# Performance work log

Hardware: AMD Instinct MI355X
Metric: run time of the kernel (lower is better)

## Reference

```python
import math
import jax, jax.numpy as jnp
import numpy as np

B, T, D_MODEL, N_HEADS = 2, 2048, 1024, 16
HEAD_DIM = D_MODEL // N_HEADS  # 64


def setup_inputs() -> dict:
    key = jax.random.key(0)
    k1, k2, k3, k4, k5 = jax.random.split(key, 5)
    x = jax.random.normal(k1, (B, T, D_MODEL), dtype=jnp.float32)
    init = 0.02
    Wq = jax.random.normal(k2, (D_MODEL, D_MODEL), dtype=jnp.float32) * init
    Wk = jax.random.normal(k3, (D_MODEL, D_MODEL), dtype=jnp.float32) * init
    Wv = jax.random.normal(k4, (D_MODEL, D_MODEL), dtype=jnp.float32) * init
    Wo = jax.random.normal(k5, (D_MODEL, D_MODEL), dtype=jnp.float32) * init
    # causal mask, broadcastable over (B, H): 1 = keep, 0 = masked
    mask = jnp.tril(jnp.ones((T, T), dtype=jnp.int32))[None, None, :, :]
    return {"x": x, "Wq": Wq, "Wk": Wk, "Wv": Wv, "Wo": Wo, "mask": mask}


def ternary_weight(W):
    # BitNet-b1.58 style ternary quantization with straight-through estimator
    scale = jnp.mean(jnp.abs(W))
    Wt = jnp.round(jnp.clip(W / (scale + 1e-8), -1.0, 1.0)) * scale
    return W + jax.lax.stop_gradient(Wt - W)


def rope_cos_sin(seq_len, dim):
    inv_freq = 1.0 / (10000.0 ** (jnp.arange(0, dim, 2, dtype=jnp.float32) / dim))
    freqs = jnp.outer(jnp.arange(seq_len, dtype=jnp.float32), inv_freq)  # [T, dim/2]
    emb = jnp.concatenate([freqs, freqs], axis=-1)  # [T, dim]
    return jnp.cos(emb)[None, None, :, :], jnp.sin(emb)[None, None, :, :]


def rotate_half(x):
    h = x.shape[-1] // 2
    return jnp.concatenate([-x[..., h:], x[..., :h]], axis=-1)


def reference(x, Wq, Wk, Wv, Wo, mask):
    Bb, Tt, C = x.shape
    H, D = N_HEADS, HEAD_DIM
    # ternary-quantized projections (bias-free)
    q = (x @ ternary_weight(Wq).T).reshape(Bb, Tt, H, D).transpose(0, 2, 1, 3)
    k = (x @ ternary_weight(Wk).T).reshape(Bb, Tt, H, D).transpose(0, 2, 1, 3)
    v = (x @ ternary_weight(Wv).T).reshape(Bb, Tt, H, D).transpose(0, 2, 1, 3)
    cos, sin = rope_cos_sin(Tt, D)  # [1,1,T,D]
    q = q * cos + rotate_half(q) * sin
    k = k * cos + rotate_half(k) * sin
    att = jnp.einsum("bhqd,bhkd->bhqk", q, k) / math.sqrt(D)
    att = jnp.where(mask == 0, -jnp.inf, att)
    att = jax.nn.softmax(att, axis=-1)  # dropout omitted (eval mode, p effectively 0)
    y = jnp.einsum("bhqk,bhkd->bhqd", att, v)
    y = y.transpose(0, 2, 1, 3).reshape(Bb, Tt, C)
    return y @ ternary_weight(Wo).T
```

## Files before the change

kernel.cpp:

```cpp
#include <hip/hip_runtime.h>
#include <math.h>

using bf16x8  = __attribute__((ext_vector_type(8))) __bf16;
using floatx4 = __attribute__((ext_vector_type(4))) float;
using ushortx8 = __attribute__((ext_vector_type(8))) unsigned short;
using ushortx4 = __attribute__((ext_vector_type(4))) unsigned short;
typedef unsigned short u16;

__device__ __forceinline__ float bf2f(u16 u) {
  unsigned int x = ((unsigned int)u) << 16;
  return __builtin_bit_cast(float, x);
}
__device__ __forceinline__ u16 f2bf(float f) {
  unsigned int x = __builtin_bit_cast(unsigned int, f);
  x += 0x7FFFu + ((x >> 16) & 1u);
  return (u16)(x >> 16);
}
__device__ __forceinline__ float fexp2(float x) { return __builtin_amdgcn_exp2f(x); }
__device__ __forceinline__ unsigned cvtpk(float lo, float hi) {
  unsigned r;
  asm("v_cvt_pk_bf16_f32 %0, %1, %2" : "=v"(r) : "v"(lo), "v"(hi));
  return r;
}

#define GLDS16(SRC, DST)                                                        \
  __builtin_amdgcn_global_load_lds((const __attribute__((address_space(1))) void*)(SRC), \
                                   (__attribute__((address_space(3))) void*)(DST), 16, 0, 0)

__global__ __launch_bounds__(256) void cvt_kernel(const float* __restrict__ x, u16* __restrict__ xb) {
  int g = (blockIdx.x * 256 + threadIdx.x) * 8;
  float4 a = *(const float4*)(x + g);
  float4 b = *(const float4*)(x + g + 4);
  ushortx8 o;
  o[0] = f2bf(a.x); o[1] = f2bf(a.y); o[2] = f2bf(a.z); o[3] = f2bf(a.w);
  o[4] = f2bf(b.x); o[5] = f2bf(b.y); o[6] = f2bf(b.z); o[7] = f2bf(b.w);
  *(ushortx8*)(xb + g) = o;
}

__global__ __launch_bounds__(256) void absum_kernel(const float* W0, const float* W1,
                                                    const float* W2, const float* W3,
                                                    float* partials) {
  const float* W = (blockIdx.y == 0) ? W0 : (blockIdx.y == 1) ? W1 : (blockIdx.y == 2) ? W2 : W3;
  int tid = threadIdx.x;
  int base = blockIdx.x * 16384 + tid;
  float s = 0.f;
#pragma unroll
  for (int i = 0; i < 64; ++i) s += fabsf(W[base + i * 256]);
  __shared__ float red[256];
  red[tid] = s;
  __syncthreads();
  for (int off = 128; off > 0; off >>= 1) {
    if (tid < off) red[tid] += red[tid + off];
    __syncthreads();
  }
  if (tid == 0) partials[blockIdx.y * 64 + blockIdx.x] = red[0];
}

__global__ void scales_kernel(const float* partials, float* scales) {
  int w = threadIdx.x;
  if (w < 4) {
    float s = 0.f;
    for (int i = 0; i < 64; ++i) s += partials[w * 64 + i];
    scales[w] = s * (1.f / 1048576.f);
  }
}

__global__ __launch_bounds__(256) void quant_kernel(const float* W0, const float* W1,
                                                    const float* W2, const float* W3,
                                                    const float* scales, u16* Wt) {
  int w = blockIdx.y;
  const float* W = (w == 0) ? W0 : (w == 1) ? W1 : (w == 2) ? W2 : W3;
  u16* O = Wt + (size_t)w * (1u << 20);
  float s = scales[w] + 1e-8f;
  int e = (blockIdx.x * 256 + threadIdx.x) * 4;
  float4 v = *(const float4*)(W + e);
  ushortx4 o;
  o[0] = f2bf(rintf(fminf(fmaxf(v.x / s, -1.f), 1.f)));
  o[1] = f2bf(rintf(fminf(fmaxf(v.y / s, -1.f), 1.f)));
  o[2] = f2bf(rintf(fminf(fmaxf(v.z / s, -1.f), 1.f)));
  o[3] = f2bf(rintf(fminf(fmaxf(v.w / s, -1.f), 1.f)));
  *(ushortx4*)(O + e) = o;
}

__global__ __launch_bounds__(256) void gemm_qkv(const u16* __restrict__ A, const u16* __restrict__ Wt,
                                                u16* __restrict__ QKV, u16* __restrict__ vt,
                                                const float* __restrict__ scales) {
  const int K = 1024;
  __shared__ __align__(16) u16 As[128][64];
  __shared__ __align__(16) u16 Bs[64][64];
  int tid = threadIdx.x;
  int wave = tid >> 6, lane = tid & 63;
  int quad = lane >> 4, l16 = lane & 15;
  int flat = blockIdx.y * 32 + blockIdx.x;
  int swz = (flat & 7) * 192 + (flat >> 3);
  int bx = swz & 31, by = swz >> 5;
  int bm = bx * 128;
  int bnc = by * 64;
  int mat = bnc >> 10, bn = bnc & 1023;
  int wm = wave * 32;
  floatx4 acc[2][4] = {};
  const u16* ga = A  + (size_t)(bm + wave * 32 + (lane >> 3)) * K + (lane & 7) * 8;
  const u16* gb = Wt + (size_t)(bnc + wave * 16 + (lane >> 3)) * K + (lane & 7) * 8;
  for (int k0 = 0; k0 < K; k0 += 64) {
    __syncthreads();
#pragma unroll
    for (int i = 0; i < 4; ++i)
      GLDS16(ga + (size_t)i * 8 * K + k0, &As[wave * 32 + i * 8][0]);
#pragma unroll
    for (int i = 0; i < 2; ++i)
      GLDS16(gb + (size_t)i * 8 * K + k0, &Bs[wave * 16 + i * 8][0]);
    __syncthreads();
#pragma unroll
    for (int kk = 0; kk < 64; kk += 32) {
      bf16x8 a[2], b[4];
#pragma unroll
      for (int i = 0; i < 2; ++i)
        a[i] = __builtin_bit_cast(bf16x8, *(const ushortx8*)&As[wm + i * 16 + l16][kk + quad * 8]);
#pragma unroll
      for (int j = 0; j < 4; ++j)
        b[j] = __builtin_bit_cast(bf16x8, *(const ushortx8*)&Bs[j * 16 + l16][kk + quad * 8]);
#pragma unroll
      for (int i = 0; i < 2; ++i)
#pragma unroll
        for (int j = 0; j < 4; ++j)
          acc[i][j] = __builtin_amdgcn_mfma_f32_16x16x32_bf16(a[i], b[j], acc[i][j], 0, 0, 0);
    }
  }
  float sc = scales[mat];
  if (mat < 2) {
    u16* outp = QKV + (size_t)mat * (4u << 20);
    float qs = (mat == 0) ? 0.125f * 1.4426950408889634f : 1.0f;
    float inv0 = exp2f(-(float)l16 * (13.287712379549449f / 32.f));
    float inv1 = exp2f(-(float)(16 + l16) * (13.287712379549449f / 32.f));
#pragma unroll
    for (int i = 0; i < 2; ++i)
#pragma unroll
      for (int rg = 0; rg < 4; ++rg) {
        int row = bm + wm + i * 16 + quad * 4 + rg;
        float tf = (float)(row & 2047);
#pragma unroll
        for (int j = 0; j < 2; ++j) {
          float ang = tf * (j ? inv1 : inv0);
          float s = __sinf(ang), c = __cosf(ang);
          float v1 = acc[i][j][rg] * sc, v2 = acc[i][j + 2][rg] * sc;
          int col = bn + j * 16 + l16;
          outp[(size_t)row * 1024 + col]      = f2bf((v1 * c - v2 * s) * qs);
          outp[(size_t)row * 1024 + col + 32] = f2bf((v2 * c + v1 * s) * qs);
        }
      }
  } else {
    int h = bn >> 6;
#pragma unroll
    for (int i = 0; i < 2; ++i) {
      int row0 = bm + wm + i * 16 + quad * 4;
      int b = row0 >> 11, t0 = row0 & 2047;
#pragma unroll
      for (int j = 0; j < 4; ++j) {
        int d = j * 16 + l16;
        ushortx4 o;
#pragma unroll
        for (int rg = 0; rg < 4; ++rg) o[rg] = f2bf(acc[i][j][rg] * sc);
        *(ushortx4*)(vt + (size_t)((b * 16 + h) * 64 + d) * 2048 + t0) = o;
      }
    }
  }
}

__global__ __launch_bounds__(256) void gemm_out(const u16* __restrict__ A, const u16* __restrict__ B,
                                                float* __restrict__ C, const float* __restrict__ scale_ptr) {
  const int K = 1024, N = 1024;
  __shared__ __align__(16) u16 As[128][64];
  __shared__ __align__(16) u16 Bs[128][64];
  int tid = threadIdx.x;
  int wave = tid >> 6, lane = tid & 63;
  int quad = lane >> 4, l16 = lane & 15;
  int bm = blockIdx.x * 128, bn = blockIdx.y * 128;
  int wm = (wave >> 1) * 64, wn = (wave & 1) * 64;
  floatx4 acc[4][4] = {};
  const u16* ga = A + (size_t)(bm + wave * 32 + (lane >> 3)) * K + (lane & 7) * 8;
  const u16* gb = B + (size_t)(bn + wave * 32 + (lane >> 3)) * K + (lane & 7) * 8;
  for (int k0 = 0; k0 < K; k0 += 64) {
    __syncthreads();
#pragma unroll
    for (int i = 0; i < 4; ++i)
      GLDS16(ga + (size_t)i * 8 * K + k0, &As[wave * 32 + i * 8][0]);
#pragma unroll
    for (int i = 0; i < 4; ++i)
      GLDS16(gb + (size_t)i * 8 * K + k0, &Bs[wave * 32 + i * 8][0]);
    __syncthreads();
#pragma unroll
    for (int kk = 0; kk < 64; kk += 32) {
      bf16x8 a[4], b[4];
#pragma unroll
      for (int i = 0; i < 4; ++i)
        a[i] = __builtin_bit_cast(bf16x8, *(const ushortx8*)&As[wm + i * 16 + l16][kk + quad * 8]);
#pragma unroll
      for (int j = 0; j < 4; ++j)
        b[j] = __builtin_bit_cast(bf16x8, *(const ushortx8*)&Bs[wn + j * 16 + l16][kk + quad * 8]);
#pragma unroll
      for (int i = 0; i < 4; ++i)
#pragma unroll
        for (int j = 0; j < 4; ++j)
          acc[i][j] = __builtin_amdgcn_mfma_f32_16x16x32_bf16(a[i], b[j], acc[i][j], 0, 0, 0);
    }
  }
  float sc = scale_ptr[0];
#pragma unroll
  for (int i = 0; i < 4; ++i)
#pragma unroll
    for (int j = 0; j < 4; ++j)
#pragma unroll
      for (int rg = 0; rg < 4; ++rg) {
        int row = bm + wm + i * 16 + quad * 4 + rg;
        int col = bn + wn + j * 16 + l16;
        C[(size_t)row * N + col] = acc[i][j][rg] * sc;
      }
}

__global__ __launch_bounds__(256, 2) void attn_kernel(const u16* __restrict__ q, const u16* __restrict__ k,
                                                      const u16* __restrict__ vt, u16* __restrict__ y) {
  __shared__ __align__(16) u16 Ks[2][64][72];
  __shared__ __align__(16) u16 Vt[2][64][72];
  __shared__ __align__(16) u16 Ps[8][16][72];
  const int T = 2048, C = 1024;
  int tid = threadIdx.x;
  int wave = tid >> 6, lane = tid & 63;
  int quad = lane >> 4, l16 = lane & 15;
  int p = blockIdx.x;
  int b = blockIdx.y >> 4, h = blockIdx.y & 15;
  int wq[2];
  wq[0] = p * 64 + wave * 16;
  wq[1] = (31 - p) * 64 + wave * 16;
  int dt[2] = {p, 31 - p};
  int nkt = 32 - p;

  bf16x8 bq[2][2];
#pragma unroll
  for (int g = 0; g < 2; ++g) {
    const u16* gq = q + (size_t)(b * T + wq[g] + l16) * C + h * 64 + quad * 8;
    bq[g][0] = __builtin_bit_cast(bf16x8, *(const ushortx8*)(gq));
    bq[g][1] = __builtin_bit_cast(bf16x8, *(const ushortx8*)(gq + 32));
  }

  ushortx8 onesu;
#pragma unroll
  for (int j = 0; j < 8; ++j) onesu[j] = 0x3F80;
  bf16x8 bones = __builtin_bit_cast(bf16x8, onesu);

  int srow = tid >> 2, sc16 = (tid & 3) << 4;
  const u16* kptr  = k  + (size_t)(b * T + srow) * C + h * 64 + sc16;
  const u16* vtptr = vt + (size_t)(blockIdx.y * 64 + srow) * 2048 + sc16;

  floatx4 o[2][5] = {};

  ushortx8 kra = *(const ushortx8*)kptr;
  ushortx8 krb = *(const ushortx8*)(kptr + 8);
  ushortx8 vra = *(const ushortx8*)vtptr;
  ushortx8 vrb = *(const ushortx8*)(vtptr + 8);
  *(ushortx8*)&Ks[0][srow][sc16]     = kra;
  *(ushortx8*)&Ks[0][srow][sc16 + 8] = krb;
  *(ushortx8*)&Vt[0][srow][sc16]     = vra;
  *(ushortx8*)&Vt[0][srow][sc16 + 8] = vrb;
  __syncthreads();

  for (int kt = 0; kt < nkt; ++kt) {
    int cur = kt & 1;
    bool haveNext = (kt + 1) < nkt;
    if (haveNext) {
      kra = *(const ushortx8*)(kptr + (size_t)(kt + 1) * 64 * C);
      krb = *(const ushortx8*)(kptr + (size_t)(kt + 1) * 64 * C + 8);
      vra = *(const ushortx8*)(vtptr + (kt + 1) * 64);
      vrb = *(const ushortx8*)(vtptr + (kt + 1) * 64 + 8);
    }

    bool act[2] = {kt <= dt[0], true};

    floatx4 sacc[2][4] = {};
#pragma unroll
    for (int nt = 0; nt < 4; ++nt) {
      bf16x8 ak0 = __builtin_bit_cast(bf16x8, *(const ushortx8*)&Ks[cur][nt * 16 + l16][quad * 8]);
      bf16x8 ak1 = __builtin_bit_cast(bf16x8, *(const ushortx8*)&Ks[cur][nt * 16 + l16][32 + quad * 8]);
#pragma unroll
      for (int g = 0; g < 2; ++g)
        if (act[g]) {
          sacc[g][nt] = __builtin_amdgcn_mfma_f32_16x16x32_bf16(ak0, bq[g][0], sacc[g][nt], 0, 0, 0);
          sacc[g][nt] = __builtin_amdgcn_mfma_f32_16x16x32_bf16(ak1, bq[g][1], sacc[g][nt], 0, 0, 0);
        }
    }

#pragma unroll
    for (int g = 0; g < 2; ++g)
      if (act[g]) {
        if (kt == dt[g]) {
          int qg = wq[g] + l16;
#pragma unroll
          for (int nt = 0; nt < 4; ++nt)
#pragma unroll
            for (int rg = 0; rg < 4; ++rg)
              if (kt * 64 + nt * 16 + quad * 4 + rg > qg) sacc[g][nt][rg] = -__builtin_inff();
        }
#pragma unroll
        for (int nt = 0; nt < 4; ++nt) {
          float p0 = fexp2(sacc[g][nt][0]);
          float p1 = fexp2(sacc[g][nt][1]);
          float p2 = fexp2(sacc[g][nt][2]);
          float p3 = fexp2(sacc[g][nt][3]);
          unsigned lo = cvtpk(p0, p1);
          unsigned hi = cvtpk(p2, p3);
          *(uint2*)&Ps[wave * 2 + g][l16][nt * 16 + quad * 4] = make_uint2(lo, hi);
        }
      }

    bf16x8 ap[2][2];
#pragma unroll
    for (int g = 0; g < 2; ++g)
      if (act[g]) {
        ap[g][0] = __builtin_bit_cast(bf16x8, *(const ushortx8*)&Ps[wave * 2 + g][l16][quad * 8]);
        ap[g][1] = __builtin_bit_cast(bf16x8, *(const ushortx8*)&Ps[wave * 2 + g][l16][32 + quad * 8]);
      }
#pragma unroll
    for (int nt = 0; nt < 4; ++nt) {
      bf16x8 bv0 = __builtin_bit_cast(bf16x8, *(const ushortx8*)&Vt[cur][nt * 16 + l16][quad * 8]);
      bf16x8 bv1 = __builtin_bit_cast(bf16x8, *(const ushortx8*)&Vt[cur][nt * 16 + l16][32 + quad * 8]);
#pragma unroll
      for (int g = 0; g < 2; ++g)
        if (act[g]) {
          o[g][nt] = __builtin_amdgcn_mfma_f32_16x16x32_bf16(ap[g][0], bv0, o[g][nt], 0, 0, 0);
          o[g][nt] = __builtin_amdgcn_mfma_f32_16x16x32_bf16(ap[g][1], bv1, o[g][nt], 0, 0, 0);
        }
    }
#pragma unroll
    for (int g = 0; g < 2; ++g)
      if (act[g]) {
        o[g][4] = __builtin_amdgcn_mfma_f32_16x16x32_bf16(ap[g][0], bones, o[g][4], 0, 0, 0);
        o[g][4] = __builtin_amdgcn_mfma_f32_16x16x32_bf16(ap[g][1], bones, o[g][4], 0, 0, 0);
      }

    if (haveNext) {
      int nb = cur ^ 1;
      *(ushortx8*)&Ks[nb][srow][sc16]     = kra;
      *(ushortx8*)&Ks[nb][srow][sc16 + 8] = krb;
      *(ushortx8*)&Vt[nb][srow][sc16]     = vra;
      *(ushortx8*)&Vt[nb][srow][sc16 + 8] = vrb;
    }
    __syncthreads();
  }

#pragma unroll
  for (int g = 0; g < 2; ++g)
#pragma unroll
    for (int nt = 0; nt < 4; ++nt)
#pragma unroll
      for (int rg = 0; rg < 4; ++rg) {
        int qg = wq[g] + quad * 4 + rg;
        int col = h * 64 + nt * 16 + l16;
        y[(size_t)(b * T + qg) * C + col] = f2bf(o[g][nt][rg] / o[g][4][rg]);
      }
}

extern "C" void kernel_launch(void* const* d_in, const int* in_sizes, int n_in,
                              void* d_out, int out_size, void* d_ws, size_t ws_size,
                              hipStream_t stream) {
  const float* x  = (const float*)d_in[0];
  const float* Wq = (const float*)d_in[1];
  const float* Wk = (const float*)d_in[2];
  const float* Wv = (const float*)d_in[3];
  const float* Wo = (const float*)d_in[4];

  char* ws = (char*)d_ws;
  float* partials = (float*)ws;
  float* scales   = (float*)(ws + 1024);
  u16* Wt  = (u16*)(ws + 4096);
  u16* xb  = (u16*)(ws + 4096 + (size_t)(8u << 20));
  u16* qb  = xb + (4u << 20);
  u16* kb  = qb + (4u << 20);
  u16* vtb = kb + (4u << 20);
  u16* yb  = vtb + (4u << 20);
  float* out = (float*)d_out;

  cvt_kernel<<<2048, 256, 0, stream>>>(x, xb);
  absum_kernel<<<dim3(64, 4), 256, 0, stream>>>(Wq, Wk, Wv, Wo, partials);
  scales_kernel<<<1, 64, 0, stream>>>(partials, scales);
  quant_kernel<<<dim3(1024, 4), 256, 0, stream>>>(Wq, Wk, Wv, Wo, scales, Wt);

  gemm_qkv<<<dim3(32, 48), 256, 0, stream>>>(xb, Wt, qb, vtb, scales);
  attn_kernel<<<dim3(16, 32), 256, 0, stream>>>(qb, kb, vtb, yb);
  gemm_out<<<dim3(32, 8), 256, 0, stream>>>(yb, Wt + 3 * (1u << 20), out, scales + 3);
}
```

Baseline: 214.8 us.

## Split attention into per-strip blocks, drop scales kernel, remove GEMM tile swizzle

The attention kernel no longer pairs a short and a long causal strip in one block. It now launches one block per 64-query strip, with heavy strips scheduled first, and raises the occupancy hint to 3 blocks per CU with a smaller P buffer. The separate scales kernel is removed: every consumer sums the 64 partials itself, which saves a launch but repeats a small reduction in every thread. The block-index swizzle in the QKV GEMM is also removed, which may hurt L2 locality.

```diff
diff --git a/kernel.cpp b/kernel.cpp
--- a/kernel.cpp
+++ b/kernel.cpp
@@ -21,6 +21,11 @@
   unsigned r;
   asm("v_cvt_pk_bf16_f32 %0, %1, %2" : "=v"(r) : "v"(lo), "v"(hi));
   return r;
+}
+__device__ __forceinline__ float scale_of(const float* __restrict__ partials, int w) {
+  float s = 0.f;
+  for (int i = 0; i < 64; ++i) s += partials[w * 64 + i];
+  return s * (1.f / 1048576.f);
 }
 
 #define GLDS16(SRC, DST)                                                        \
@@ -56,22 +61,13 @@
   if (tid == 0) partials[blockIdx.y * 64 + blockIdx.x] = red[0];
 }
 
-__global__ void scales_kernel(const float* partials, float* scales) {
-  int w = threadIdx.x;
-  if (w < 4) {
-    float s = 0.f;
-    for (int i = 0; i < 64; ++i) s += partials[w * 64 + i];
-    scales[w] = s * (1.f / 1048576.f);
-  }
-}
-
 __global__ __launch_bounds__(256) void quant_kernel(const float* W0, const float* W1,
                                                     const float* W2, const float* W3,
-                                                    const float* scales, u16* Wt) {
+                                                    const float* partials, u16* Wt) {
   int w = blockIdx.y;
   const float* W = (w == 0) ? W0 : (w == 1) ? W1 : (w == 2) ? W2 : W3;
   u16* O = Wt + (size_t)w * (1u << 20);
-  float s = scales[w] + 1e-8f;
+  float s = scale_of(partials, w) + 1e-8f;
   int e = (blockIdx.x * 256 + threadIdx.x) * 4;
   float4 v = *(const float4*)(W + e);
   ushortx4 o;
@@ -84,18 +80,15 @@
 
 __global__ __launch_bounds__(256) void gemm_qkv(const u16* __restrict__ A, const u16* __restrict__ Wt,
                                                 u16* __restrict__ QKV, u16* __restrict__ vt,
-                                                const float* __restrict__ scales) {
+                                                const float* __restrict__ partials) {
   const int K = 1024;
   __shared__ __align__(16) u16 As[128][64];
   __shared__ __align__(16) u16 Bs[64][64];
   int tid = threadIdx.x;
   int wave = tid >> 6, lane = tid & 63;
   int quad = lane >> 4, l16 = lane & 15;
-  int flat = blockIdx.y * 32 + blockIdx.x;
-  int swz = (flat & 7) * 192 + (flat >> 3);
-  int bx = swz & 31, by = swz >> 5;
-  int bm = bx * 128;
-  int bnc = by * 64;
+  int bm = blockIdx.x * 128;
+  int bnc = blockIdx.y * 64;
   int mat = bnc >> 10, bn = bnc & 1023;
   int wm = wave * 32;
   floatx4 acc[2][4] = {};
@@ -126,7 +119,7 @@
           acc[i][j] = __builtin_amdgcn_mfma_f32_16x16x32_bf16(a[i], b[j], acc[i][j], 0, 0, 0);
     }
   }
-  float sc = scales[mat];
+  float sc = scale_of(partials, mat);
   if (mat < 2) {
     u16* outp = QKV + (size_t)mat * (4u << 20);
     float qs = (mat == 0) ? 0.125f * 1.4426950408889634f : 1.0f;
@@ -167,7 +160,7 @@
 }
 
 __global__ __launch_bounds__(256) void gemm_out(const u16* __restrict__ A, const u16* __restrict__ B,
-                                                float* __restrict__ C, const float* __restrict__ scale_ptr) {
+                                                float* __restrict__ C, const float* __restrict__ partials) {
   const int K = 1024, N = 1024;
   __shared__ __align__(16) u16 As[128][64];
   __shared__ __align__(16) u16 Bs[128][64];
@@ -204,7 +197,7 @@
           acc[i][j] = __builtin_amdgcn_mfma_f32_16x16x32_bf16(a[i], b[j], acc[i][j], 0, 0, 0);
     }
   }
-  float sc = scale_ptr[0];
+  float sc = scale_of(partials, 3);
 #pragma unroll
   for (int i = 0; i < 4; ++i)
 #pragma unroll
@@ -217,29 +210,25 @@
       }
 }
 
-__global__ __launch_bounds__(256, 2) void attn_kernel(const u16* __restrict__ q, const u16* __restrict__ k,
+__global__ __launch_bounds__(256, 3) void attn_kernel(const u16* __restrict__ q, const u16* __restrict__ k,
                                                       const u16* __restrict__ vt, u16* __restrict__ y) {
   __shared__ __align__(16) u16 Ks[2][64][72];
   __shared__ __align__(16) u16 Vt[2][64][72];
-  __shared__ __align__(16) u16 Ps[8][16][72];
+  __shared__ __align__(16) u16 Ps[4][16][72];
   const int T = 2048, C = 1024;
   int tid = threadIdx.x;
   int wave = tid >> 6, lane = tid & 63;
   int quad = lane >> 4, l16 = lane & 15;
-  int p = blockIdx.x;
+  int strip = 31 - blockIdx.x;
   int b = blockIdx.y >> 4, h = blockIdx.y & 15;
-  int wq[2];
-  wq[0] = p * 64 + wave * 16;
-  wq[1] = (31 - p) * 64 + wave * 16;
-  int dt[2] = {p, 31 - p};
-  int nkt = 32 - p;
-
-  bf16x8 bq[2][2];
-#pragma unroll
-  for (int g = 0; g < 2; ++g) {
-    const u16* gq = q + (size_t)(b * T + wq[g] + l16) * C + h * 64 + quad * 8;
-    bq[g][0] = __builtin_bit_cast(bf16x8, *(const ushortx8*)(gq));
-    bq[g][1] = __builtin_bit_cast(bf16x8, *(const ushortx8*)(gq + 32));
+  int wq = strip * 64 + wave * 16;
+  int nkt = strip + 1;
+
+  bf16x8 bq0, bq1;
+  {
+    const u16* gq = q + (size_t)(b * T + wq + l16) * C + h * 64 + quad * 8;
+    bq0 = __builtin_bit_cast(bf16x8, *(const ushortx8*)(gq));
+    bq1 = __builtin_bit_cast(bf16x8, *(const ushortx8*)(gq + 32));
   }
 
   ushortx8 onesu;
@@ -251,7 +240,7 @@
   const u16* kptr  = k  + (size_t)(b * T + srow) * C + h * 64 + sc16;
   const u16* vtptr = vt + (size_t)(blockIdx.y * 64 + srow) * 2048 + sc16;
 
-  floatx4 o[2][5] = {};
+  floatx4 o[5] = {};
 
   ushortx8 kra = *(const ushortx8*)kptr;
   ushortx8 krb = *(const ushortx8*)(kptr + 8);
@@ -273,68 +262,45 @@
       vrb = *(const ushortx8*)(vtptr + (kt + 1) * 64 + 8);
     }
 
-    bool act[2] = {kt <= dt[0], true};
-
-    floatx4 sacc[2][4] = {};
+    floatx4 sacc[4] = {};
 #pragma unroll
     for (int nt = 0; nt < 4; ++nt) {
       bf16x8 ak0 = __builtin_bit_cast(bf16x8, *(const ushortx8*)&Ks[cur][nt * 16 + l16][quad * 8]);
       bf16x8 ak1 = __builtin_bit_cast(bf16x8, *(const ushortx8*)&Ks[cur][nt * 16 + l16][32 + quad * 8]);
-#pragma unroll
-      for (int g = 0; g < 2; ++g)
-        if (act[g]) {
-          sacc[g][nt] = __builtin_amdgcn_mfma_f32_16x16x32_bf16(ak0, bq[g][0], sacc[g][nt], 0, 0, 0);
-          sacc[g][nt] = __builtin_amdgcn_mfma_f32_16x16x32_bf16(ak1, bq[g][1], sacc[g][nt], 0, 0, 0);
-        }
-    }
-
-#pragma unroll
-    for (int g = 0; g < 2; ++g)
-      if (act[g]) {
-        if (kt == dt[g]) {
-          int qg = wq[g] + l16;
-#pragma unroll
-          for (int nt = 0; nt < 4; ++nt)
-#pragma unroll
-            for (int rg = 0; rg < 4; ++rg)
-              if (kt * 64 + nt * 16 + quad * 4 + rg > qg) sacc[g][nt][rg] = -__builtin_inff();
-        }
-#pragma unroll
-        for (int nt = 0; nt < 4; ++nt) {
-          float p0 = fexp2(sacc[g][nt][0]);
-          float p1 = fexp2(sacc[g][nt][1]);
-          float p2 = fexp2(sacc[g][nt][2]);
-          float p3 = fexp2(sacc[g][nt][3]);
-          unsigned lo = cvtpk(p0, p1);
-          unsigned hi = cvtpk(p2, p3);
-          *(uint2*)&Ps[wave * 2 + g][l16][nt * 16 + quad * 4] = make_uint2(lo, hi);
-        }
-      }
-
-    bf16x8 ap[2][2];
-#pragma unroll
-    for (int g = 0; g < 2; ++g)
-      if (act[g]) {
-        ap[g][0] = __builtin_bit_cast(bf16x8, *(const ushortx8*)&Ps[wave * 2 + g][l16][quad * 8]);
-        ap[g][1] = __builtin_bit_cast(bf16x8, *(const ushortx8*)&Ps[wave * 2 + g][l16][32 + quad * 8]);
-      }
+      sacc[nt] = __builtin_amdgcn_mfma_f32_16x16x32_bf16(ak0, bq0, sacc[nt], 0, 0, 0);
+      sacc[nt] = __builtin_amdgcn_mfma_f32_16x16x32_bf16(ak1, bq1, sacc[nt], 0, 0, 0);
+    }
+
+    if (kt == strip) {
+      int qg = wq + l16;
+#pragma unroll
+      for (int nt = 0; nt < 4; ++nt)
+#pragma unroll
+        for (int rg = 0; rg < 4; ++rg)
+          if (kt * 64 + nt * 16 + quad * 4 + rg > qg) sacc[nt][rg] = -__builtin_inff();
+    }
+#pragma unroll
+    for (int nt = 0; nt < 4; ++nt) {
+      float p0 = fexp2(sacc[nt][0]);
+      float p1 = fexp2(sacc[nt][1]);
+      float p2 = fexp2(sacc[nt][2]);
+      float p3 = fexp2(sacc[nt][3]);
+      unsigned lo = cvtpk(p0, p1);
+      unsigned hi = cvtpk(p2, p3);
+      *(uint2*)&Ps[wave][l16][nt * 16 + quad * 4] = make_uint2(lo, hi);
+    }
+
+    bf16x8 ap0 = __builtin_bit_cast(bf16x8, *(const ushortx8*)&Ps[wave][l16][quad * 8]);
+    bf16x8 ap1 = __builtin_bit_cast(bf16x8, *(const ushortx8*)&Ps[wave][l16][32 + quad * 8]);
 #pragma unroll
     for (int nt = 0; nt < 4; ++nt) {
       bf16x8 bv0 = __builtin_bit_cast(bf16x8, *(const ushortx8*)&Vt[cur][nt * 16 + l16][quad * 8]);
       bf16x8 bv1 = __builtin_bit_cast(bf16x8, *(const ushortx8*)&Vt[cur][nt * 16 + l16][32 + quad * 8]);
-#pragma unroll
-      for (int g = 0; g < 2; ++g)
-        if (act[g]) {
-          o[g][nt] = __builtin_amdgcn_mfma_f32_16x16x32_bf16(ap[g][0], bv0, o[g][nt], 0, 0, 0);
-          o[g][nt] = __builtin_amdgcn_mfma_f32_16x16x32_bf16(ap[g][1], bv1, o[g][nt], 0, 0, 0);
-        }
-    }
-#pragma unroll
-    for (int g = 0; g < 2; ++g)
-      if (act[g]) {
-        o[g][4] = __builtin_amdgcn_mfma_f32_16x16x32_bf16(ap[g][0], bones, o[g][4], 0, 0, 0);
-        o[g][4] = __builtin_amdgcn_mfma_f32_16x16x32_bf16(ap[g][1], bones, o[g][4], 0, 0, 0);
-      }
+      o[nt] = __builtin_amdgcn_mfma_f32_16x16x32_bf16(ap0, bv0, o[nt], 0, 0, 0);
+      o[nt] = __builtin_amdgcn_mfma_f32_16x16x32_bf16(ap1, bv1, o[nt], 0, 0, 0);
+    }
+    o[4] = __builtin_amdgcn_mfma_f32_16x16x32_bf16(ap0, bones, o[4], 0, 0, 0);
+    o[4] = __builtin_amdgcn_mfma_f32_16x16x32_bf16(ap1, bones, o[4], 0, 0, 0);
 
     if (haveNext) {
       int nb = cur ^ 1;
@@ -347,15 +313,13 @@
   }
 
 #pragma unroll
-  for (int g = 0; g < 2; ++g)
-#pragma unroll
-    for (int nt = 0; nt < 4; ++nt)
-#pragma unroll
-      for (int rg = 0; rg < 4; ++rg) {
-        int qg = wq[g] + quad * 4 + rg;
-        int col = h * 64 + nt * 16 + l16;
-        y[(size_t)(b * T + qg) * C + col] = f2bf(o[g][nt][rg] / o[g][4][rg]);
-      }
+  for (int nt = 0; nt < 4; ++nt)
+#pragma unroll
+    for (int rg = 0; rg < 4; ++rg) {
+      int qg = wq + quad * 4 + rg;
+      int col = h * 64 + nt * 16 + l16;
+      y[(size_t)(b * T + qg) * C + col] = f2bf(o[nt][rg] / o[4][rg]);
+    }
 }
 
 extern "C" void kernel_launch(void* const* d_in, const int* in_sizes, int n_in,
@@ -369,7 +333,6 @@
 
   char* ws = (char*)d_ws;
   float* partials = (float*)ws;
-  float* scales   = (float*)(ws + 1024);
   u16* Wt  = (u16*)(ws + 4096);
   u16* xb  = (u16*)(ws + 4096 + (size_t)(8u << 20));
   u16* qb  = xb + (4u << 20);
@@ -380,10 +343,9 @@
 
   cvt_kernel<<<2048, 256, 0, stream>>>(x, xb);
   absum_kernel<<<dim3(64, 4), 256, 0, stream>>>(Wq, Wk, Wv, Wo, partials);
-  scales_kernel<<<1, 64, 0, stream>>>(partials, scales);
-  quant_kernel<<<dim3(1024, 4), 256, 0, stream>>>(Wq, Wk, Wv, Wo, scales, Wt);
-
-  gemm_qkv<<<dim3(32, 48), 256, 0, stream>>>(xb, Wt, qb, vtb, scales);
-  attn_kernel<<<dim3(16, 32), 256, 0, stream>>>(qb, kb, vtb, yb);
-  gemm_out<<<dim3(32, 8), 256, 0, stream>>>(yb, Wt + 3 * (1u << 20), out, scales + 3);
-}
+  quant_kernel<<<dim3(1024, 4), 256, 0, stream>>>(Wq, Wk, Wv, Wo, partials, Wt);
+
+  gemm_qkv<<<dim3(32, 48), 256, 0, stream>>>(xb, Wt, qb, vtb, partials);
+  attn_kernel<<<dim3(32, 32), 256, 0, stream>>>(qb, kb, vtb, yb);
+  gemm_out<<<dim3(32, 8), 256, 0, stream>>>(yb, Wt + 3 * (1u << 20), out, partials);
+}
```

New measurement: 234.4 us. 9.1% more time.
